# Optimization experiments

Hardware: AMD Instinct MI355X
Metric: run time of the kernel (lower is better)

The kernel has to match this reference:

```python
import jax, jax.numpy as jnp
import numpy as np

N, D = 16384, 256

def setup_inputs() -> dict:
    key = jax.random.key(0)
    k1, k2, k3 = jax.random.split(key, 3)
    X = jax.random.normal(k1, (N, D), dtype=jnp.float32)
    W = jax.random.normal(k2, (D, D), dtype=jnp.float32) * (1.0 / np.sqrt(D))
    b = jax.random.normal(k3, (D,), dtype=jnp.float32) * (1.0 / np.sqrt(D))
    return {"X": X, "W": W, "b": b}

def reference(X, W, b):
    # Step 1: bilinear attention A = X W X^T   (N, N) -- materialized as in original
    A = (X @ W) @ X.T
    # Step 2: context aggregation Z = A X      (N, D)
    Z = A @ X
    # Step 3: output head g = Z b              (N,)
    g = Z @ b
    return g
```

## Files before the change

kernel.cpp:

```cpp
#include <hip/hip_runtime.h>

#define NROWS 16384
#define DDIM  256

__global__ __launch_bounds__(256) void k1_v(const float* __restrict__ X,
                                            const float* __restrict__ b,
                                            float* __restrict__ v) {
    const int tid  = threadIdx.x;
    const int lane = tid & 63;
    const int wave = tid >> 6;
    const int bid  = blockIdx.x;

    const float4* X4 = (const float4*)X;
    const float4  bf = ((const float4*)b)[lane];

    float4 vacc = make_float4(0.f, 0.f, 0.f, 0.f);
    const int row0 = bid * 32 + wave * 8;
    #pragma unroll
    for (int i = 0; i < 8; ++i) {
        const int r = row0 + i;
        const float4 x = X4[r * 64 + lane];
        float t = x.x * bf.x + x.y * bf.y + x.z * bf.z + x.w * bf.w;
        #pragma unroll
        for (int off = 32; off; off >>= 1) t += __shfl_xor(t, off, 64);
        vacc.x += t * x.x;
        vacc.y += t * x.y;
        vacc.z += t * x.z;
        vacc.w += t * x.w;
    }

    __shared__ float sp[4][DDIM];
    ((float4*)sp[wave])[lane] = vacc;
    __syncthreads();
    const float s = sp[0][tid] + sp[1][tid] + sp[2][tid] + sp[3][tid];
    atomicAdd(&v[tid], s);
}

__global__ __launch_bounds__(256) void k2_w2(const float* __restrict__ W,
                                             const float* __restrict__ v,
                                             float* __restrict__ w2) {
    const int tid  = threadIdx.x;
    const int lane = tid & 63;
    const int wave = tid >> 6;
    const int row  = blockIdx.x * 4 + wave;

    const float4 vf = ((const float4*)v)[lane];
    const float4 w  = ((const float4*)W)[row * 64 + lane];
    float t = w.x * vf.x + w.y * vf.y + w.z * vf.z + w.w * vf.w;
    #pragma unroll
    for (int off = 32; off; off >>= 1) t += __shfl_xor(t, off, 64);
    if (lane == 0) w2[row] = t;
}

__global__ __launch_bounds__(256) void k3_g(const float* __restrict__ X,
                                            const float* __restrict__ w2,
                                            float* __restrict__ g) {
    const int tid  = threadIdx.x;
    const int lane = tid & 63;
    const int wave = tid >> 6;
    const int bid  = blockIdx.x;

    const float4* X4 = (const float4*)X;
    const float4  wf = ((const float4*)w2)[lane];

    const int row0 = bid * 32 + wave * 8;
    #pragma unroll
    for (int i = 0; i < 8; ++i) {
        const int r = row0 + i;
        const float4 x = X4[r * 64 + lane];
        float t = x.x * wf.x + x.y * wf.y + x.z * wf.z + x.w * wf.w;
        #pragma unroll
        for (int off = 32; off; off >>= 1) t += __shfl_xor(t, off, 64);
        if (lane == 0) g[r] = t;
    }
}

extern "C" void kernel_launch(void* const* d_in, const int* in_sizes, int n_in,
                              void* d_out, int out_size, void* d_ws, size_t ws_size,
                              hipStream_t stream) {
    const float* X = (const float*)d_in[0];
    const float* W = (const float*)d_in[1];
    const float* b = (const float*)d_in[2];
    float* out = (float*)d_out;

    float* v  = (float*)d_ws;
    float* w2 = v + DDIM;

    hipMemsetAsync(v, 0, DDIM * sizeof(float), stream);
    k1_v <<<512, 256, 0, stream>>>(X, b, v);
    k2_w2<<< 64, 256, 0, stream>>>(W, v, w2);
    k3_g <<<512, 256, 0, stream>>>(X, w2, out);
}
```

Before: 86.91 us.

## Fuse three kernels into one cooperative kernel with grid syncs and slotted atomics

New measurement: 188.8 us. +117.3%, slower.

```diff
diff --git a/kernel.cpp b/kernel.cpp
--- a/kernel.cpp
+++ b/kernel.cpp
@@ -1,77 +1,75 @@
 #include <hip/hip_runtime.h>
+#include <hip/hip_cooperative_groups.h>
 
-#define NROWS 16384
+namespace cg = cooperative_groups;
+
 #define DDIM  256
+#define NSLOT 64
 
-__global__ __launch_bounds__(256) void k1_v(const float* __restrict__ X,
-                                            const float* __restrict__ b,
-                                            float* __restrict__ v) {
+__global__ __launch_bounds__(256) void fused_g(const float* __restrict__ X,
+                                               const float* __restrict__ W,
+                                               const float* __restrict__ b,
+                                               float* __restrict__ g,
+                                               float* __restrict__ vslots,
+                                               float* __restrict__ w2) {
+    cg::grid_group grid = cg::this_grid();
     const int tid  = threadIdx.x;
     const int lane = tid & 63;
     const int wave = tid >> 6;
     const int bid  = blockIdx.x;
+    const float4* X4 = (const float4*)X;
 
-    const float4* X4 = (const float4*)X;
-    const float4  bf = ((const float4*)b)[lane];
+    {
+        const float4 bf = ((const float4*)b)[lane];
+        float4 vacc = make_float4(0.f, 0.f, 0.f, 0.f);
+        const int row0 = bid * 32 + wave * 8;
+        #pragma unroll
+        for (int i = 0; i < 8; ++i) {
+            const float4 x = X4[(row0 + i) * 64 + lane];
+            float t = x.x * bf.x + x.y * bf.y + x.z * bf.z + x.w * bf.w;
+            #pragma unroll
+            for (int off = 32; off; off >>= 1) t += __shfl_xor(t, off, 64);
+            vacc.x += t * x.x; vacc.y += t * x.y;
+            vacc.z += t * x.z; vacc.w += t * x.w;
+        }
+        __shared__ float sp[4][DDIM];
+        ((float4*)sp[wave])[lane] = vacc;
+        __syncthreads();
+        const float s = sp[0][tid] + sp[1][tid] + sp[2][tid] + sp[3][tid];
+        atomicAdd(&vslots[(bid & (NSLOT - 1)) * DDIM + tid], s);
+    }
+    __threadfence();
+    grid.sync();
 
-    float4 vacc = make_float4(0.f, 0.f, 0.f, 0.f);
-    const int row0 = bid * 32 + wave * 8;
-    #pragma unroll
-    for (int i = 0; i < 8; ++i) {
-        const int r = row0 + i;
-        const float4 x = X4[r * 64 + lane];
-        float t = x.x * bf.x + x.y * bf.y + x.z * bf.z + x.w * bf.w;
+    if (bid < NSLOT) {
+        float s = 0.f;
+        #pragma unroll 8
+        for (int j = 0; j < NSLOT; ++j) s += vslots[j * DDIM + tid];
+        __shared__ __align__(16) float sv[DDIM];
+        sv[tid] = s;
+        __syncthreads();
+        const float4 vf = ((const float4*)sv)[lane];
+        const int row = bid * 4 + wave;
+        const float4 w = ((const float4*)W)[row * 64 + lane];
+        float t = w.x * vf.x + w.y * vf.y + w.z * vf.z + w.w * vf.w;
         #pragma unroll
         for (int off = 32; off; off >>= 1) t += __shfl_xor(t, off, 64);
-        vacc.x += t * x.x;
-        vacc.y += t * x.y;
-        vacc.z += t * x.z;
-        vacc.w += t * x.w;
+        if (lane == 0) w2[row] = t;
+        __threadfence();
     }
+    grid.sync();
 
-    __shared__ float sp[4][DDIM];
-    ((float4*)sp[wave])[lane] = vacc;
-    __syncthreads();
-    const float s = sp[0][tid] + sp[1][tid] + sp[2][tid] + sp[3][tid];
-    atomicAdd(&v[tid], s);
-}
-
-__global__ __launch_bounds__(256) void k2_w2(const float* __restrict__ W,
-                                             const float* __restrict__ v,
-                                             float* __restrict__ w2) {
-    const int tid  = threadIdx.x;
-    const int lane = tid & 63;
-    const int wave = tid >> 6;
-    const int row  = blockIdx.x * 4 + wave;
-
-    const float4 vf = ((const float4*)v)[lane];
-    const float4 w  = ((const float4*)W)[row * 64 + lane];
-    float t = w.x * vf.x + w.y * vf.y + w.z * vf.z + w.w * vf.w;
-    #pragma unroll
-    for (int off = 32; off; off >>= 1) t += __shfl_xor(t, off, 64);
-    if (lane == 0) w2[row] = t;
-}
-
-__global__ __launch_bounds__(256) void k3_g(const float* __restrict__ X,
-                                            const float* __restrict__ w2,
-                                            float* __restrict__ g) {
-    const int tid  = threadIdx.x;
-    const int lane = tid & 63;
-    const int wave = tid >> 6;
-    const int bid  = blockIdx.x;
-
-    const float4* X4 = (const float4*)X;
-    const float4  wf = ((const float4*)w2)[lane];
-
-    const int row0 = bid * 32 + wave * 8;
-    #pragma unroll
-    for (int i = 0; i < 8; ++i) {
-        const int r = row0 + i;
-        const float4 x = X4[r * 64 + lane];
-        float t = x.x * wf.x + x.y * wf.y + x.z * wf.z + x.w * wf.w;
+    {
+        const float4 wf = ((const float4*)w2)[lane];
+        const int row0 = bid * 32 + wave * 8;
         #pragma unroll
-        for (int off = 32; off; off >>= 1) t += __shfl_xor(t, off, 64);
-        if (lane == 0) g[r] = t;
+        for (int i = 0; i < 8; ++i) {
+            const float4 x = X4[(row0 + i) * 64 + lane];
+            float t = x.x * wf.x + x.y * wf.y + x.z * wf.z + x.w * wf.w;
+            #pragma unroll
+            for (int off = 32; off; off >>= 1) t += __shfl_xor(t, off, 64);
+            if (lane == 0) g[row0 + i] = t;
+        }
     }
 }
 
@@ -83,11 +81,13 @@
     const float* b = (const float*)d_in[2];
     float* out = (float*)d_out;
 
-    float* v  = (float*)d_ws;
-    float* w2 = v + DDIM;
+    float* vslots = (float*)d_ws;
+    float* w2     = vslots + NSLOT * DDIM;
 
-    hipMemsetAsync(v, 0, DDIM * sizeof(float), stream);
-    k1_v <<<512, 256, 0, stream>>>(X, b, v);
-    k2_w2<<< 64, 256, 0, stream>>>(W, v, w2);
-    k3_g <<<512, 256, 0, stream>>>(X, w2, out);
+    hipMemsetAsync(vslots, 0, NSLOT * DDIM * sizeof(float), stream);
+
+    void* args[] = { (void*)&X, (void*)&W, (void*)&b,
+                     (void*)&out, (void*)&vslots, (void*)&w2 };
+    hipLaunchCooperativeKernel(reinterpret_cast<void*>(fused_g),
+                               dim3(512), dim3(256), args, 0, stream);
 }
```
